# Performance work log

Measured on AMD Instinct MI355X. Metric: run time of the kernel, lower is better.

The kernel has to match this reference:

```python
import jax, jax.numpy as jnp
import numpy as np

B, S, D = 2, 2048, 1024
H, DH = 16, 64  # num_head, head_dim; H*DH == D


def setup_inputs() -> dict:
    key = jax.random.key(0)
    ks = jax.random.split(key, 10)
    stdv = 1.0 / np.sqrt(D)
    def lin(k):
        kw, kb = jax.random.split(k)
        W = jax.random.uniform(kw, (D, D), jnp.float32, -stdv, stdv)
        b = jax.random.uniform(kb, (D,), jnp.float32, -stdv, stdv)
        return W, b
    Wq, bq = lin(ks[0]); Wk, bk = lin(ks[1]); Wv, bv = lin(ks[2]); Wo, bo = lin(ks[3])
    x = jax.random.normal(ks[4], (B, S, D), jnp.float32)
    # causal mask: True = attend
    mask = jnp.tril(jnp.ones((S, S), jnp.bool_))
    mask = jnp.broadcast_to(mask, (B, S, S))
    return {"x": x, "mask": mask, "Wq": Wq, "bq": bq, "Wk": Wk, "bk": bk,
            "Wv": Wv, "bv": bv, "Wo": Wo, "bo": bo}


def _split_head(t):
    # [B,S,D] -> [B*H, S, DH]
    return t.reshape(B, S, H, DH).transpose(0, 2, 1, 3).reshape(B * H, S, DH)


def _concat_head(t):
    # [B*H, S, DH] -> [B, S, D]
    return t.reshape(B, H, S, DH).transpose(0, 2, 1, 3).reshape(B, S, D)


def reference(x, mask, Wq, bq, Wk, bk, Wv, bv, Wo, bo):
    q = _split_head(x @ Wq.T + bq)
    k = _split_head(x @ Wk.T + bk)
    v = _split_head(x @ Wv.T + bv)
    scale = 1.0 / jnp.sqrt(jnp.float32(DH))
    # scores: [B, H, S, S], masked softmax (flash-attention math, unfused ref)
    scores = jnp.einsum('nqd,nkd->nqk', q, k).reshape(B, H, S, S) * scale
    scores = jnp.where(mask[:, None, :, :], scores, jnp.finfo(scores.dtype).min)
    attn = jax.nn.softmax(scores, axis=-1)
    out = jnp.einsum('bhqk,nkd->bhqd', attn, v.reshape(B, H, S, DH).reshape(B * H, S, DH)).reshape(B * H, S, DH) if False else jnp.einsum('nqk,nkd->nqd', attn.reshape(B * H, S, S), v)
    return _concat_head(out) @ Wo.T + bo
```

## Files before the change

kernel.cpp:

```cpp
#include <hip/hip_runtime.h>
#include <cstdint>

#define S_LEN  2048
#define NH     16
#define DHEAD  64
#define DMODEL 1024

typedef __bf16 bf16x8 __attribute__((ext_vector_type(8)));
typedef __bf16 bf16x2 __attribute__((ext_vector_type(2)));
typedef float  f32x4  __attribute__((ext_vector_type(4)));
typedef float  f32x16 __attribute__((ext_vector_type(16)));

__device__ __forceinline__ unsigned short f2bf(float x) {
  union { float f; unsigned int u; } c; c.f = x;
  unsigned int u = c.u;
  return (unsigned short)((u + 0x7fffu + ((u >> 16) & 1u)) >> 16);
}

__device__ __forceinline__ unsigned int pkbf(float a, float b) {
#if __has_builtin(__builtin_amdgcn_cvt_pk_bf16_f32)
  bf16x2 r = __builtin_amdgcn_cvt_pk_bf16_f32(a, b);
  return *(unsigned int*)&r;
#else
  return (unsigned int)f2bf(a) | ((unsigned int)f2bf(b) << 16);
#endif
}

__device__ __forceinline__ unsigned short f2bf1(float x) {
#if __has_builtin(__builtin_amdgcn_cvt_pk_bf16_f32)
  bf16x2 r = __builtin_amdgcn_cvt_pk_bf16_f32(x, x);
  union { bf16x2 v; unsigned int u; } c; c.v = r;
  return (unsigned short)(c.u & 0xffffu);
#else
  return f2bf(x);
#endif
}

__device__ __forceinline__ __bf16 us2bf(unsigned short u) {
  union { unsigned short u; __bf16 b; } c; c.u = u; return c.b;
}

__device__ __forceinline__ void glds16(const void* g, void* l) {
  __builtin_amdgcn_global_load_lds(
      (const __attribute__((address_space(1))) void*)g,
      (__attribute__((address_space(3))) void*)l, 16, 0, 0);
}

__device__ __forceinline__ f32x4 mfma16(bf16x8 a, bf16x8 b, f32x4 c) {
  return __builtin_amdgcn_mfma_f32_16x16x32_bf16(a, b, c, 0, 0, 0);
}

__device__ __forceinline__ f32x16 mfma32(bf16x8 a, bf16x8 b, f32x16 c) {
  return __builtin_amdgcn_mfma_f32_32x32x16_bf16(a, b, c, 0, 0, 0);
}

__device__ __forceinline__ void plswap(unsigned int &a, unsigned int &b) {
#if __has_builtin(__builtin_amdgcn_permlane32_swap)
  typedef unsigned int uint2v __attribute__((ext_vector_type(2)));
  uint2v r = __builtin_amdgcn_permlane32_swap(a, b, false, false);
  a = r[0]; b = r[1];
#else
  asm("v_permlane32_swap_b32 %0, %1" : "+v"(a), "+v"(b));
#endif
}

__global__ void cvt_all(const float* __restrict__ x,
                        const float* __restrict__ Wq,
                        const float* __restrict__ Wk,
                        const float* __restrict__ Wv,
                        const float* __restrict__ Wo,
                        unsigned short* __restrict__ xb,
                        unsigned short* __restrict__ wqkv,
                        unsigned short* __restrict__ wo) {
  const int b = blockIdx.x;
  const float* src;
  unsigned short* dst;
  int off;
  if (b < 4096)      { src = x;  dst = xb;                off = b; }
  else if (b < 5120) { src = Wq; dst = wqkv;              off = b - 4096; }
  else if (b < 6144) { src = Wk; dst = wqkv + (1 << 20);  off = b - 5120; }
  else if (b < 7168) { src = Wv; dst = wqkv + (2 << 20);  off = b - 6144; }
  else               { src = Wo; dst = wo;                off = b - 7168; }
  const int i = (off * 256 + threadIdx.x) * 4;
  float4 v = *(const float4*)&src[i];
  uint2 r;
  r.x = pkbf(v.x, v.y);
  r.y = pkbf(v.z, v.w);
  *(uint2*)&dst[i] = r;
}

template<int MODE, int BN>
__global__ __launch_bounds__(256)
void gemm_bt(const unsigned short* __restrict__ A,
             const unsigned short* __restrict__ W,
             const float* __restrict__ bias0,
             const float* __restrict__ bias1,
             const float* __restrict__ bias2,
             unsigned short* __restrict__ Qt,
             unsigned short* __restrict__ Kb,
             unsigned short* __restrict__ Vt,
             float* __restrict__ Out,
             int K) {
  constexpr int JN = BN / 32;
  __shared__ __align__(16) unsigned short As[2][128 * 32];
  __shared__ __align__(16) unsigned short Bs[2][BN * 32];
  const int t    = threadIdx.x;
  const int lane = t & 63;
  const int w    = t >> 6;
  const int lr   = lane & 15, lq = lane >> 4;
  const int wm   = (w >> 1) * 64, wn = (w & 1) * (BN / 2);
  const int m0   = blockIdx.y * 128, n0 = blockIdx.x * BN;
  const int ra   = t >> 2, ca = (t & 3) * 8;

  f32x4 acc[4][JN] = {};

  const int niter = K >> 6;
  for (int kk = 0; kk < niter; ++kk) {
    const int k0 = kk << 6;
#pragma unroll
    for (int kh = 0; kh < 2; ++kh) {
      const int kc = k0 + kh * 32;
      glds16(A + (m0 + ra) * K + kc + ca,      &As[kh][ra * 32 + ca]);
      glds16(A + (m0 + 64 + ra) * K + kc + ca, &As[kh][(64 + ra) * 32 + ca]);
      glds16(W + (n0 + ra) * K + kc + ca,      &Bs[kh][ra * 32 + ca]);
      if (BN == 128)
        glds16(W + (n0 + 64 + ra) * K + kc + ca, &Bs[kh][(64 + ra) * 32 + ca]);
    }
    __syncthreads();
#pragma unroll
    for (int kh = 0; kh < 2; ++kh) {
      bf16x8 af[4], bg[JN];
#pragma unroll
      for (int i = 0; i < 4; ++i)
        af[i] = *(const bf16x8*)&As[kh][(wm + i * 16 + lr) * 32 + lq * 8];
#pragma unroll
      for (int j = 0; j < JN; ++j)
        bg[j] = *(const bf16x8*)&Bs[kh][(wn + j * 16 + lr) * 32 + lq * 8];
#pragma unroll
      for (int i = 0; i < 4; ++i)
#pragma unroll
        for (int j = 0; j < JN; ++j)
          acc[i][j] = mfma16(af[i], bg[j], acc[i][j]);
    }
    __syncthreads();
  }

  if (MODE == 0) {
    const int tsel = n0 >> 10;
#pragma unroll
    for (int i = 0; i < 4; ++i) {
#pragma unroll
      for (int j = 0; j < JN; ++j) {
        const int mb = m0 + wm + i * 16 + lq * 4;
        const int n  = n0 + wn + j * 16 + lr;
        const int d  = n & 1023;
        const int bidx = mb >> 11, s = mb & (S_LEN - 1);
        const int h = d >> 6, dh = d & 63;
        const int bh = bidx * NH + h;
        const float bv0 = (tsel == 0) ? bias0[d] : ((tsel == 1) ? bias1[d] : bias2[d]);
        if (tsel == 0) {
          const float sc = 0.125f * 1.44269504088896f;
#pragma unroll
          for (int r = 0; r < 4; ++r)
            Qt[(bh * S_LEN + s + r) * DHEAD + dh] = f2bf1((acc[i][j][r] + bv0) * sc);
        } else if (tsel == 2) {
          uint2 pv;
          pv.x = pkbf(acc[i][j][0] + bv0, acc[i][j][1] + bv0);
          pv.y = pkbf(acc[i][j][2] + bv0, acc[i][j][3] + bv0);
          *(uint2*)&Vt[(bh * DHEAD + dh) * S_LEN + s] = pv;
        } else {
#pragma unroll
          for (int r = 0; r < 4; ++r)
            Kb[(bh * S_LEN + s + r) * DHEAD + dh] = f2bf1(acc[i][j][r] + bv0);
        }
      }
    }
  } else {
#pragma unroll
    for (int i = 0; i < 4; ++i)
#pragma unroll
      for (int j = 0; j < JN; ++j)
#pragma unroll
        for (int r = 0; r < 4; ++r) {
          const int m = m0 + wm + i * 16 + lq * 4 + r;
          const int n = n0 + wn + j * 16 + lr;
          Out[m * DMODEL + n] = acc[i][j][r] + bias0[n];
        }
  }
}

__global__ __launch_bounds__(256, 2)
void flash_kernel(const unsigned short* __restrict__ Qt,
                  const unsigned short* __restrict__ Kb,
                  const unsigned short* __restrict__ Vt,
                  unsigned short* __restrict__ Ocat) {
  __shared__ __align__(16) unsigned short Ks[2][2][64 * 64];
  __shared__ __align__(16) unsigned short Vs[2][2][64 * 64];
  __shared__ float MlS[2][32];
  const int w = threadIdx.x >> 6, lane = threadIdx.x & 63;
  const int l31 = lane & 31, half = lane >> 5;
  const int qh = w & 1, sub = w >> 1;
  const int bh = blockIdx.x;
  const int pp = blockIdx.y;
  const char* Kc = (const char*)(Kb + bh * (S_LEN * DHEAD));
  const char* Vc = (const char*)(Vt + bh * (DHEAD * S_LEN));
  const unsigned short* Qp = Qt + bh * (S_LEN * DHEAD);
  const int bb = bh >> 4, hd = bh & 15;

  bf16x8 ones;
#pragma unroll
  for (int j = 0; j < 8; ++j) ones[j] = (__bf16)1.0f;

  auto run_strip = [&](int sb) {
    const int len = sb + 1;
    const int nit = (len + 1) >> 1;
    const int q0 = sb * 64;
    const int qa = q0 + qh * 32 + l31;
    bf16x8 qf[4];
#pragma unroll
    for (int d = 0; d < 4; ++d)
      qf[d] = *(const bf16x8*)&Qp[qa * 64 + d * 16 + half * 8];
    f32x16 o0 = {}, o1 = {}, lacc = {};

    auto stage = [&](int buf, int it) {
#pragma unroll
      for (int s2 = 0; s2 < 2; ++s2) {
        const int kt = 2 * it + s2;
#pragma unroll
        for (int h8 = 0; h8 < 2; ++h8) {
          const int rb = w * 16 + h8 * 8;
          const int r  = rb + (lane >> 3);
          const int gs = (lane & 7) ^ (r & 7) ^ ((r >> 3) & 3);
          glds16(Kc + (kt * 64 + r) * 128 + gs * 16, &Ks[buf][s2][rb * 64]);
          glds16(Vc + r * 4096 + kt * 128 + gs * 16, &Vs[buf][s2][rb * 64]);
        }
      }
    };

    stage(0, 0);
    if (nit > 1) stage(1, 1);
    for (int it = 0; it < nit; ++it) {
      const int buf = it & 1;
      if (it + 1 < nit) asm volatile("s_waitcnt vmcnt(8)" ::: "memory");
      else              asm volatile("s_waitcnt vmcnt(0)" ::: "memory");
      __builtin_amdgcn_s_barrier();
      __builtin_amdgcn_sched_barrier(0);
      const int kt = 2 * it + sub;
      if (kt < len) {
        const unsigned short* Kt = &Ks[buf][sub][0];
        const unsigned short* Vl = &Vs[buf][sub][0];
        const int r0 = l31, r1 = 32 + l31;
        const int x0 = (r0 & 7) ^ ((r0 >> 3) & 3);
        const int x1 = (r1 & 7) ^ ((r1 >> 3) & 3);
        f32x16 st0 = {}, st1 = {};
#pragma unroll
        for (int d = 0; d < 4; ++d) {
          const int sl = d * 2 + half;
          st0 = mfma32(*(const bf16x8*)&Kt[r0 * 64 + ((sl ^ x0) << 3)], qf[d], st0);
          st1 = mfma32(*(const bf16x8*)&Kt[r1 * 64 + ((sl ^ x1) << 3)], qf[d], st1);
        }
        const bool diag = (kt == sb);
        unsigned int pk0[8], pk1[8];
#pragma unroll
        for (int m = 0; m < 8; ++m) {
          const int rA = 2 * m, rB = 2 * m + 1;
          const int kA = (rA & 3) + 8 * (rA >> 2) + 4 * half;
          const int kB = (rB & 3) + 8 * (rB >> 2) + 4 * half;
          float e0 = __builtin_amdgcn_exp2f(st0[rA]);
          float e1 = __builtin_amdgcn_exp2f(st0[rB]);
          float f0 = __builtin_amdgcn_exp2f(st1[rA]);
          float f1 = __builtin_amdgcn_exp2f(st1[rB]);
          if (diag) {
            e0 = (kt * 64 + kA > qa) ? 0.f : e0;
            e1 = (kt * 64 + kB > qa) ? 0.f : e1;
            f0 = (kt * 64 + 32 + kA > qa) ? 0.f : f0;
            f1 = (kt * 64 + 32 + kB > qa) ? 0.f : f1;
          }
          pk0[m] = pkbf(e0, e1);
          pk1[m] = pkbf(f0, f1);
        }
#pragma unroll
        for (int s = 0; s < 4; ++s) {
          unsigned int u, u2, v, v2;
          if (s == 0)      { u = pk0[0]; u2 = pk0[1]; v = pk0[2]; v2 = pk0[3]; }
          else if (s == 1) { u = pk0[4]; u2 = pk0[5]; v = pk0[6]; v2 = pk0[7]; }
          else if (s == 2) { u = pk1[0]; u2 = pk1[1]; v = pk1[2]; v2 = pk1[3]; }
          else             { u = pk1[4]; u2 = pk1[5]; v = pk1[6]; v2 = pk1[7]; }
          plswap(u, v);
          plswap(u2, v2);
          union { unsigned int ui[4]; bf16x8 bv; } pf;
          pf.ui[0] = u; pf.ui[1] = u2; pf.ui[2] = v; pf.ui[3] = v2;
          const int sl = s * 2 + half;
          o0 = mfma32(*(const bf16x8*)&Vl[r0 * 64 + ((sl ^ x0) << 3)], pf.bv, o0);
          o1 = mfma32(*(const bf16x8*)&Vl[r1 * 64 + ((sl ^ x1) << 3)], pf.bv, o1);
          lacc = mfma32(ones, pf.bv, lacc);
        }
      }
      __builtin_amdgcn_s_barrier();
      __builtin_amdgcn_sched_barrier(0);
      if (it + 2 < nit) stage(buf, it + 2);
    }

    float* Mo = (float*)&Ks[1 - ((nit - 1) & 1)][0][0];
    const int qrow = qh * 32 + l31;
    if (sub == 1) {
      if (lane < 32) MlS[qh][l31] = lacc[0];
#pragma unroll
      for (int g = 0; g < 4; ++g) {
        const int sl0 = 2 * g + half;
        const int sl1 = 8 + 2 * g + half;
        f32x4 s0 = { o0[4 * g], o0[4 * g + 1], o0[4 * g + 2], o0[4 * g + 3] };
        f32x4 s1 = { o1[4 * g], o1[4 * g + 1], o1[4 * g + 2], o1[4 * g + 3] };
        *(f32x4*)&Mo[qrow * 64 + ((sl0 ^ (qrow & 15)) << 2)] = s0;
        *(f32x4*)&Mo[qrow * 64 + ((sl1 ^ (qrow & 15)) << 2)] = s1;
      }
    }
    __syncthreads();
    if (sub == 0) {
      const float inv = 1.f / (lacc[0] + MlS[qh][l31]);
      unsigned short* Or = Ocat + (bb * S_LEN + q0 + qrow) * DMODEL + hd * DHEAD;
#pragma unroll
      for (int g = 0; g < 4; ++g) {
        const int sl0 = 2 * g + half;
        const int sl1 = 8 + 2 * g + half;
        const f32x4 m0 = *(const f32x4*)&Mo[qrow * 64 + ((sl0 ^ (qrow & 15)) << 2)];
        const f32x4 m1 = *(const f32x4*)&Mo[qrow * 64 + ((sl1 ^ (qrow & 15)) << 2)];
        uint2 ov0, ov1;
        ov0.x = pkbf((o0[4 * g]     + m0[0]) * inv, (o0[4 * g + 1] + m0[1]) * inv);
        ov0.y = pkbf((o0[4 * g + 2] + m0[2]) * inv, (o0[4 * g + 3] + m0[3]) * inv);
        ov1.x = pkbf((o1[4 * g]     + m1[0]) * inv, (o1[4 * g + 1] + m1[1]) * inv);
        ov1.y = pkbf((o1[4 * g + 2] + m1[2]) * inv, (o1[4 * g + 3] + m1[3]) * inv);
        *(uint2*)&Or[8 * g + 4 * half]      = ov0;
        *(uint2*)&Or[32 + 8 * g + 4 * half] = ov1;
      }
    }
    __syncthreads();
  };

  run_strip(31 - pp);
  run_strip(pp);
}

extern "C" void kernel_launch(void* const* d_in, const int* in_sizes, int n_in,
                              void* d_out, int out_size, void* d_ws, size_t ws_size,
                              hipStream_t stream) {
  const float* x  = (const float*)d_in[0];
  const float* Wq = (const float*)d_in[2];
  const float* bq = (const float*)d_in[3];
  const float* Wk = (const float*)d_in[4];
  const float* bk = (const float*)d_in[5];
  const float* Wv = (const float*)d_in[6];
  const float* bv = (const float*)d_in[7];
  const float* Wo = (const float*)d_in[8];
  const float* bo = (const float*)d_in[9];
  float* out = (float*)d_out;

  char* ws = (char*)d_ws;
  unsigned short* xb   = (unsigned short*)(ws);
  unsigned short* wqkv = (unsigned short*)(ws + (8ull  << 20));
  unsigned short* wo   = (unsigned short*)(ws + (14ull << 20));
  unsigned short* Qt   = (unsigned short*)(ws + (16ull << 20));
  unsigned short* Kb   = (unsigned short*)(ws + (24ull << 20));
  unsigned short* Vt   = (unsigned short*)(ws + (32ull << 20));
  unsigned short* Ocat = (unsigned short*)(ws + (40ull << 20));

  cvt_all<<<8192, 256, 0, stream>>>(x, Wq, Wk, Wv, Wo, xb, wqkv, wo);

  gemm_bt<0, 128><<<dim3(24, 32), 256, 0, stream>>>(xb, wqkv, bq, bk, bv,
                                                    Qt, Kb, Vt, nullptr, 1024);
  flash_kernel<<<dim3(32, 16), 256, 0, stream>>>(Qt, Kb, Vt, Ocat);
  gemm_bt<1, 64><<<dim3(16, 32), 256, 0, stream>>>(Ocat, wo, bo, nullptr, nullptr,
                                                   nullptr, nullptr, nullptr, out, 1024);
}
```

Measured before the change: 196.1 us.

## Add 256x256-tile 8-wave QKV GEMM with interleaved staging; simplify flash prefetch

Replaces the QKV projection GEMM with a new 512-thread kernel that computes 256x256 output tiles. It uses swizzled LDS double buffering via global-to-LDS loads and interleaves the next tile's staging with MFMA phases under raised wave priority. A block-index swizzle is added for cache locality. The larger tiles are meant to raise arithmetic intensity and cut redundant global loads. Separately, the flash kernel's two-ahead prefetch with explicit vmcnt waits becomes a simpler one-ahead prefetch behind __syncthreads, which may expose more load latency.

```diff
diff --git a/kernel.cpp b/kernel.cpp
--- a/kernel.cpp
+++ b/kernel.cpp
@@ -89,16 +89,141 @@
   *(uint2*)&dst[i] = r;
 }
 
+__global__ __launch_bounds__(512, 2)
+void gemm8(const unsigned short* __restrict__ A,
+           const unsigned short* __restrict__ W,
+           const float* __restrict__ bias0,
+           const float* __restrict__ bias1,
+           const float* __restrict__ bias2,
+           unsigned short* __restrict__ Qt,
+           unsigned short* __restrict__ Kb,
+           unsigned short* __restrict__ Vt) {
+  __shared__ __align__(16) unsigned short As[2][2][128 * 64];
+  __shared__ __align__(16) unsigned short Bs[2][2][128 * 64];
+  const int t = threadIdx.x, l = t & 63, w = t >> 6;
+  const int lr = l & 15, lq = l >> 4;
+  const int bid = blockIdx.x;
+  const int swz = (bid & 7) * 24 + (bid >> 3);
+  const int bx = swz % 12, by = swz / 12;
+  const int m0 = by * 256, n0 = bx * 256;
+  const int wm2 = w >> 2, wn4 = w & 3;
+  const int srow = l >> 3, sslot = l & 7;
+
+  f32x4 acc[8][4] = {};
+
+  auto stgA = [&](int buf, int half, int kt, int j) {
+    const int r  = (w + 8 * j) * 8 + srow;
+    const int gs = sslot ^ (r & 7);
+    glds16(A + (m0 + half * 128 + r) * 1024 + kt * 64 + gs * 8,
+           &As[buf][half][r * 64 + sslot * 8]);
+  };
+  auto stgB = [&](int buf, int half, int kt, int j) {
+    const int r  = (w + 8 * j) * 8 + srow;
+    const int gs = sslot ^ (r & 7);
+    glds16(W + (n0 + half * 128 + r) * 1024 + kt * 64 + gs * 8,
+           &Bs[buf][half][r * 64 + sslot * 8]);
+  };
+  auto ldA = [&](int buf, int mi, int kk) -> bf16x8 {
+    const int rr = mi * 16 + lr;
+    const int sl = (kk * 4 + lq) ^ (rr & 7);
+    return *(const bf16x8*)&As[buf][wm2][rr * 64 + sl * 8];
+  };
+  auto ldB = [&](int buf, int nj, int kk) -> bf16x8 {
+    const int rr = (wn4 & 1) * 64 + nj * 16 + lr;
+    const int sl = (kk * 4 + lq) ^ (rr & 7);
+    return *(const bf16x8*)&Bs[buf][wn4 >> 1][rr * 64 + sl * 8];
+  };
+
+#pragma unroll
+  for (int j = 0; j < 2; ++j) stgB(0, 0, 0, j);
+#pragma unroll
+  for (int j = 0; j < 2; ++j) stgB(0, 1, 0, j);
+#pragma unroll
+  for (int j = 0; j < 2; ++j) stgA(0, 0, 0, j);
+#pragma unroll
+  for (int j = 0; j < 2; ++j) stgA(0, 1, 0, j);
+#pragma unroll
+  for (int j = 0; j < 2; ++j) stgB(1, 0, 1, j);
+#pragma unroll
+  for (int j = 0; j < 2; ++j) stgB(1, 1, 1, j);
+
+  const int nkt = 16;
+  for (int kt = 0; kt < nkt; ++kt) {
+    const int buf = kt & 1;
+    if (kt + 1 < nkt) asm volatile("s_waitcnt vmcnt(4)" ::: "memory");
+    else              asm volatile("s_waitcnt vmcnt(0)" ::: "memory");
+    __builtin_amdgcn_s_barrier();
+    __builtin_amdgcn_sched_barrier(0);
+
+    bf16x8 bg[4][2];
+#pragma unroll
+    for (int nj = 0; nj < 4; ++nj) {
+      bg[nj][0] = ldB(buf, nj, 0);
+      bg[nj][1] = ldB(buf, nj, 1);
+    }
+
+    auto phase = [&](int q) {
+      const bf16x8 a00 = ldA(buf, 2 * q, 0),     a01 = ldA(buf, 2 * q, 1);
+      const bf16x8 a10 = ldA(buf, 2 * q + 1, 0), a11 = ldA(buf, 2 * q + 1, 1);
+      __builtin_amdgcn_s_setprio(1);
+#pragma unroll
+      for (int nj = 0; nj < 4; ++nj) {
+        acc[2 * q][nj]     = mfma16(a00, bg[nj][0], acc[2 * q][nj]);
+        acc[2 * q][nj]     = mfma16(a01, bg[nj][1], acc[2 * q][nj]);
+        acc[2 * q + 1][nj] = mfma16(a10, bg[nj][0], acc[2 * q + 1][nj]);
+        acc[2 * q + 1][nj] = mfma16(a11, bg[nj][1], acc[2 * q + 1][nj]);
+      }
+      __builtin_amdgcn_s_setprio(0);
+    };
+
+    if (kt + 1 < nkt) { stgA(buf ^ 1, 0, kt + 1, 0); stgA(buf ^ 1, 0, kt + 1, 1); }
+    phase(0);
+    if (kt + 1 < nkt) { stgA(buf ^ 1, 1, kt + 1, 0); stgA(buf ^ 1, 1, kt + 1, 1); }
+    phase(1);
+    __builtin_amdgcn_s_barrier();
+    __builtin_amdgcn_sched_barrier(0);
+    if (kt + 2 < nkt) { stgB(buf, 0, kt + 2, 0); stgB(buf, 0, kt + 2, 1); }
+    phase(2);
+    if (kt + 2 < nkt) { stgB(buf, 1, kt + 2, 0); stgB(buf, 1, kt + 2, 1); }
+    phase(3);
+  }
+
+  const int tsel = n0 >> 10;
+#pragma unroll
+  for (int mi = 0; mi < 8; ++mi) {
+#pragma unroll
+    for (int nj = 0; nj < 4; ++nj) {
+      const int mb = m0 + wm2 * 128 + mi * 16 + lq * 4;
+      const int n  = n0 + wn4 * 64 + nj * 16 + lr;
+      const int d  = n & 1023;
+      const int bidx = mb >> 11, s = mb & (S_LEN - 1);
+      const int h = d >> 6, dh = d & 63;
+      const int bh = bidx * NH + h;
+      const float bv0 = (tsel == 0) ? bias0[d] : ((tsel == 1) ? bias1[d] : bias2[d]);
+      if (tsel == 0) {
+        const float sc = 0.125f * 1.44269504088896f;
+#pragma unroll
+        for (int r = 0; r < 4; ++r)
+          Qt[(bh * S_LEN + s + r) * DHEAD + dh] = f2bf1((acc[mi][nj][r] + bv0) * sc);
+      } else if (tsel == 2) {
+        uint2 pv;
+        pv.x = pkbf(acc[mi][nj][0] + bv0, acc[mi][nj][1] + bv0);
+        pv.y = pkbf(acc[mi][nj][2] + bv0, acc[mi][nj][3] + bv0);
+        *(uint2*)&Vt[(bh * DHEAD + dh) * S_LEN + s] = pv;
+      } else {
+#pragma unroll
+        for (int r = 0; r < 4; ++r)
+          Kb[(bh * S_LEN + s + r) * DHEAD + dh] = f2bf1(acc[mi][nj][r] + bv0);
+      }
+    }
+  }
+}
+
 template<int MODE, int BN>
 __global__ __launch_bounds__(256)
 void gemm_bt(const unsigned short* __restrict__ A,
              const unsigned short* __restrict__ W,
              const float* __restrict__ bias0,
-             const float* __restrict__ bias1,
-             const float* __restrict__ bias2,
-             unsigned short* __restrict__ Qt,
-             unsigned short* __restrict__ Kb,
-             unsigned short* __restrict__ Vt,
              float* __restrict__ Out,
              int K) {
   constexpr int JN = BN / 32;
@@ -145,48 +270,16 @@
     __syncthreads();
   }
 
-  if (MODE == 0) {
-    const int tsel = n0 >> 10;
-#pragma unroll
-    for (int i = 0; i < 4; ++i) {
-#pragma unroll
-      for (int j = 0; j < JN; ++j) {
-        const int mb = m0 + wm + i * 16 + lq * 4;
-        const int n  = n0 + wn + j * 16 + lr;
-        const int d  = n & 1023;
-        const int bidx = mb >> 11, s = mb & (S_LEN - 1);
-        const int h = d >> 6, dh = d & 63;
-        const int bh = bidx * NH + h;
-        const float bv0 = (tsel == 0) ? bias0[d] : ((tsel == 1) ? bias1[d] : bias2[d]);
-        if (tsel == 0) {
-          const float sc = 0.125f * 1.44269504088896f;
-#pragma unroll
-          for (int r = 0; r < 4; ++r)
-            Qt[(bh * S_LEN + s + r) * DHEAD + dh] = f2bf1((acc[i][j][r] + bv0) * sc);
-        } else if (tsel == 2) {
-          uint2 pv;
-          pv.x = pkbf(acc[i][j][0] + bv0, acc[i][j][1] + bv0);
-          pv.y = pkbf(acc[i][j][2] + bv0, acc[i][j][3] + bv0);
-          *(uint2*)&Vt[(bh * DHEAD + dh) * S_LEN + s] = pv;
-        } else {
-#pragma unroll
-          for (int r = 0; r < 4; ++r)
-            Kb[(bh * S_LEN + s + r) * DHEAD + dh] = f2bf1(acc[i][j][r] + bv0);
-        }
-      }
-    }
-  } else {
-#pragma unroll
-    for (int i = 0; i < 4; ++i)
-#pragma unroll
-      for (int j = 0; j < JN; ++j)
-#pragma unroll
-        for (int r = 0; r < 4; ++r) {
-          const int m = m0 + wm + i * 16 + lq * 4 + r;
-          const int n = n0 + wn + j * 16 + lr;
-          Out[m * DMODEL + n] = acc[i][j][r] + bias0[n];
-        }
-  }
+#pragma unroll
+  for (int i = 0; i < 4; ++i)
+#pragma unroll
+    for (int j = 0; j < JN; ++j)
+#pragma unroll
+      for (int r = 0; r < 4; ++r) {
+        const int m = m0 + wm + i * 16 + lq * 4 + r;
+        const int n = n0 + wn + j * 16 + lr;
+        Out[m * DMODEL + n] = acc[i][j][r] + bias0[n];
+      }
 }
 
 __global__ __launch_bounds__(256, 2)
@@ -238,13 +331,10 @@
     };
 
     stage(0, 0);
-    if (nit > 1) stage(1, 1);
     for (int it = 0; it < nit; ++it) {
       const int buf = it & 1;
-      if (it + 1 < nit) asm volatile("s_waitcnt vmcnt(8)" ::: "memory");
-      else              asm volatile("s_waitcnt vmcnt(0)" ::: "memory");
-      __builtin_amdgcn_s_barrier();
-      __builtin_amdgcn_sched_barrier(0);
+      __syncthreads();
+      if (it + 1 < nit) stage(1 - buf, it + 1);
       const int kt = 2 * it + sub;
       if (kt < len) {
         const unsigned short* Kt = &Ks[buf][sub][0];
@@ -296,9 +386,6 @@
           lacc = mfma32(ones, pf.bv, lacc);
         }
       }
-      __builtin_amdgcn_s_barrier();
-      __builtin_amdgcn_sched_barrier(0);
-      if (it + 2 < nit) stage(buf, it + 2);
     }
 
     float* Mo = (float*)&Ks[1 - ((nit - 1) & 1)][0][0];
@@ -366,9 +453,7 @@
 
   cvt_all<<<8192, 256, 0, stream>>>(x, Wq, Wk, Wv, Wo, xb, wqkv, wo);
 
-  gemm_bt<0, 128><<<dim3(24, 32), 256, 0, stream>>>(xb, wqkv, bq, bk, bv,
-                                                    Qt, Kb, Vt, nullptr, 1024);
+  gemm8<<<192, 512, 0, stream>>>(xb, wqkv, bq, bk, bv, Qt, Kb, Vt);
   flash_kernel<<<dim3(32, 16), 256, 0, stream>>>(Qt, Kb, Vt, Ocat);
-  gemm_bt<1, 64><<<dim3(16, 32), 256, 0, stream>>>(Ocat, wo, bo, nullptr, nullptr,
-                                                   nullptr, nullptr, nullptr, out, 1024);
-}
+  gemm_bt<1, 64><<<dim3(16, 32), 256, 0, stream>>>(Ocat, wo, bo, out, 1024);
+}
```

Result: slower. 210.9 us (+7.5%).
